# Optimization experiments

Hardware: AMD Instinct MI355X
Metric: run time of the kernel (lower is better)

Reference implementation:

```python
import jax, jax.numpy as jnp
import numpy as np

ALPHA = 1.0
GAMMA = 2.0
SMOOTH = 1e-07
B, S = 8192, 4096


def setup_inputs() -> dict:
    key = jax.random.key(0)
    k1, k2, k3, k4 = jax.random.split(key, 4)
    scores = jax.random.normal(k1, (B, S), dtype=jnp.float32)
    head_position = jax.random.randint(k2, (B,), 0, S, dtype=jnp.int64) if jax.config.jax_enable_x64 else jax.random.randint(k2, (B,), 0, S).astype(jnp.int32)
    tail_position = jax.random.randint(k3, (B,), 0, S).astype(head_position.dtype)
    score_mask = jax.random.randint(k4, (B, S), 0, 2, dtype=jnp.int32)
    return {"scores": scores, "head_position": head_position,
            "tail_position": tail_position, "score_mask": score_mask}


def reference(scores, head_position, tail_position, score_mask):
    # scores: [B, S] float; head/tail_position: [B] int; score_mask: [B, S] int
    batch_size = scores.shape[0]
    bidx = jnp.arange(batch_size)
    # exclude head and tail positions from the negative set
    m = score_mask.at[bidx, head_position].set(-1)
    m = m.at[bidx, tail_position].set(-1)
    neg = (m == 1)  # [B, S] candidate negatives
    # positive score per sample, broadcast against all candidates
    pos = jnp.take_along_axis(scores, tail_position[:, None], axis=1)  # [B, 1]
    # log_softmax over the pair [pos, neg_j] at index 0 == -softplus(neg - pos)
    logpt = -jax.nn.softplus(scores - pos)  # [B, S]
    pt = jnp.clip(jnp.exp(logpt), SMOOTH, 1.0 - SMOOTH)
    fl = -ALPHA * jnp.power(1.0 - pt, GAMMA) * logpt  # [B, S] per-pair focal loss
    negf = neg.astype(scores.dtype)
    cnt = negf.sum(axis=1)  # [B] number of negatives
    # per-sample focal_loss is the MEAN over its pairs; samples with 0 negs skipped
    per_sample = jnp.where(cnt > 0, (fl * negf).sum(axis=1) / jnp.maximum(cnt, 1.0), 0.0)
    return per_sample.sum() / batch_size
```

## Files before the change

### kernel.cpp

```cpp
#include <hip/hip_runtime.h>


__device__ __forceinline__ float focal_term(float x) {
    const float e  = __expf(x);
    const float t  = 1.f + e;
    const float sp = __logf(t);
    float pt = __builtin_amdgcn_rcpf(t);
    pt = fminf(fmaxf(pt, 1e-7f), 1.f - 1e-7f);
    const float om = 1.f - pt;
    return om * om * sp;
}

template <int S>
__global__ __launch_bounds__(256, 8) void focal_row_kernel(
    const float* __restrict__ scores,
    const int*   __restrict__ head_pos,
    const int*   __restrict__ tail_pos,
    const int*   __restrict__ mask,
    float*       __restrict__ row_out,
    int B)
{
    const int lane = threadIdx.x & 63;
    const int row  = blockIdx.x * 4 + (threadIdx.x >> 6);
    if (row >= B) return;

    const int head = head_pos[row];
    const int tail = tail_pos[row];
    const float* srow = scores + (size_t)row * S;
    const int*   mrow = mask   + (size_t)row * S;
    const float4* s4 = reinterpret_cast<const float4*>(srow);
    const int4*   m4 = reinterpret_cast<const int4*>(mrow);
    const float pos = srow[tail];

    constexpr int NIT   = S / 4 / 64;
    constexpr int DEPTH = 4;
    static_assert(NIT >= DEPTH && NIT % 4 == 0, "shape");

    float4 sbuf[DEPTH];
    int4   mbuf[DEPTH];
    #pragma unroll
    for (int i = 0; i < DEPTH; ++i) {
        sbuf[i] = s4[lane + 64 * i];
        mbuf[i] = m4[lane + 64 * i];
    }

    float fsum = 0.f;
    float cnt  = 0.f;

    #pragma unroll
    for (int i = 0; i < NIT; ++i) {
        const float4 sv = sbuf[i & (DEPTH - 1)];
        const int4   mv = mbuf[i & (DEPTH - 1)];
        if (i + DEPTH < NIT) {
            sbuf[i & (DEPTH - 1)] = s4[lane + 64 * (i + DEPTH)];
            mbuf[i & (DEPTH - 1)] = m4[lane + 64 * (i + DEPTH)];
        }
        const float se[4] = {sv.x, sv.y, sv.z, sv.w};
        const int   me[4] = {mv.x, mv.y, mv.z, mv.w};
        #pragma unroll
        for (int k = 0; k < 4; ++k) {
            const float fl = focal_term(se[k] - pos);
            const float on = (me[k] == 1) ? 1.f : 0.f;
            fsum += fl * on;
            cnt  += on;
        }
    }

    #pragma unroll
    for (int off = 32; off; off >>= 1) {
        fsum += __shfl_down(fsum, off, 64);
        cnt  += __shfl_down(cnt,  off, 64);
    }

    if (lane == 0) {
        if (mrow[head] == 1) { fsum -= focal_term(srow[head] - pos); cnt -= 1.f; }
        if (tail != head && mrow[tail] == 1) { fsum -= focal_term(0.f); cnt -= 1.f; }
        row_out[row] = (cnt > 0.f) ? fsum / cnt : 0.f;
    }
}

__global__ __launch_bounds__(256) void focal_row_generic(
    const float* __restrict__ scores,
    const int*   __restrict__ head_pos,
    const int*   __restrict__ tail_pos,
    const int*   __restrict__ mask,
    float*       __restrict__ row_out,
    int S)
{
    const int row  = blockIdx.x;
    const int tid  = threadIdx.x;
    const int head = head_pos[row];
    const int tail = tail_pos[row];
    const float* srow = scores + (size_t)row * S;
    const int*   mrow = mask   + (size_t)row * S;
    const float pos = srow[tail];
    float fsum = 0.f; float cnt = 0.f;
    for (int idx = tid; idx < S; idx += 256) {
        const float fl = focal_term(srow[idx] - pos);
        const bool isneg = (mrow[idx] == 1) && (idx != head) && (idx != tail);
        if (isneg) { fsum += fl; cnt += 1.f; }
    }
    #pragma unroll
    for (int off = 32; off; off >>= 1) {
        fsum += __shfl_down(fsum, off, 64);
        cnt  += __shfl_down(cnt,  off, 64);
    }
    __shared__ float sf[4]; __shared__ float sc[4];
    const int wave = tid >> 6;
    if ((tid & 63) == 0) { sf[wave] = fsum; sc[wave] = cnt; }
    __syncthreads();
    if (tid == 0) {
        float tot = sf[0] + sf[1] + sf[2] + sf[3];
        float c   = sc[0] + sc[1] + sc[2] + sc[3];
        row_out[row] = (c > 0.f) ? tot / c : 0.f;
    }
}

__global__ __launch_bounds__(256) void final_reduce_kernel(
    const float* __restrict__ row_out, float* __restrict__ out, int B)
{
    float sum = 0.f;
    const float4* r4 = reinterpret_cast<const float4*>(row_out);
    const int nvec = B >> 2;
    for (int i = threadIdx.x; i < nvec; i += 256) {
        float4 v = r4[i];
        sum += (v.x + v.y) + (v.z + v.w);
    }
    #pragma unroll
    for (int off = 32; off; off >>= 1) sum += __shfl_down(sum, off, 64);
    __shared__ float sf[4];
    const int wave = threadIdx.x >> 6;
    if ((threadIdx.x & 63) == 0) sf[wave] = sum;
    __syncthreads();
    if (threadIdx.x == 0) out[0] = (sf[0] + sf[1] + sf[2] + sf[3]) / (float)B;
}

extern "C" void kernel_launch(void* const* d_in, const int* in_sizes, int n_in,
                              void* d_out, int out_size, void* d_ws, size_t ws_size,
                              hipStream_t stream)
{
    const float* scores = (const float*)d_in[0];
    const int*   headp  = (const int*)d_in[1];
    const int*   tailp  = (const int*)d_in[2];
    const int*   maskp  = (const int*)d_in[3];
    const int B = in_sizes[1];
    const int S = in_sizes[0] / B;

    float* rowbuf = (float*)d_ws;
    float* out    = (float*)d_out;

    if (S == 4096) {
        const int grid = (B + 3) / 4;
        focal_row_kernel<4096><<<grid, 256, 0, stream>>>(scores, headp, tailp, maskp, rowbuf, B);
    } else {
        focal_row_generic<<<B, 256, 0, stream>>>(scores, headp, tailp, maskp, rowbuf, S);
    }
    final_reduce_kernel<<<1, 256, 0, stream>>>(rowbuf, out, B);
}
```

Baseline: 288.2 us.

## Stream row tiles into LDS with direct global-to-LDS loads, double-buffered

Replaces the per-lane register prefetch ring with double-buffered global_load_lds transfers into per-wave shared-memory tiles. Explicit vmcnt/lgkmcnt waits and a sched_barrier keep the loads overlapped with compute. It also drops the pt clamp and turns the mask compare into a float convert plus fma, trimming ALU work per element. In exchange it adds LDS traffic and manual wait management, and the mask conversion is only correct when mask values are exactly 0 or 1.

```diff
diff --git a/kernel.cpp b/kernel.cpp
--- a/kernel.cpp
+++ b/kernel.cpp
@@ -1,12 +1,16 @@
 #include <hip/hip_runtime.h>
 
+
+#define GLL(gaddr, laddr)                                                          \
+    __builtin_amdgcn_global_load_lds(                                              \
+        (const __attribute__((address_space(1))) void*)(gaddr),                    \
+        (__attribute__((address_space(3))) void*)(laddr), 16, 0, 0)
 
 __device__ __forceinline__ float focal_term(float x) {
     const float e  = __expf(x);
     const float t  = 1.f + e;
     const float sp = __logf(t);
-    float pt = __builtin_amdgcn_rcpf(t);
-    pt = fminf(fmaxf(pt, 1e-7f), 1.f - 1e-7f);
+    const float pt = __builtin_amdgcn_rcpf(t);
     const float om = 1.f - pt;
     return om * om * sp;
 }
@@ -20,49 +24,52 @@
     float*       __restrict__ row_out,
     int B)
 {
+    constexpr int NIT = S / 256;
+    static_assert(S % 256 == 0 && NIT >= 4, "shape");
+
+    __shared__ float s_lds[4][2][256];
+    __shared__ int   m_lds[4][2][256];
+
     const int lane = threadIdx.x & 63;
-    const int row  = blockIdx.x * 4 + (threadIdx.x >> 6);
+    const int wid  = threadIdx.x >> 6;
+    const int row  = blockIdx.x * 4 + wid;
     if (row >= B) return;
 
     const int head = head_pos[row];
     const int tail = tail_pos[row];
     const float* srow = scores + (size_t)row * S;
     const int*   mrow = mask   + (size_t)row * S;
-    const float4* s4 = reinterpret_cast<const float4*>(srow);
-    const int4*   m4 = reinterpret_cast<const int4*>(mrow);
     const float pos = srow[tail];
 
-    constexpr int NIT   = S / 4 / 64;
-    constexpr int DEPTH = 4;
-    static_assert(NIT >= DEPTH && NIT % 4 == 0, "shape");
+    asm volatile("s_waitcnt vmcnt(0) lgkmcnt(0)" ::: "memory");
 
-    float4 sbuf[DEPTH];
-    int4   mbuf[DEPTH];
-    #pragma unroll
-    for (int i = 0; i < DEPTH; ++i) {
-        sbuf[i] = s4[lane + 64 * i];
-        mbuf[i] = m4[lane + 64 * i];
-    }
+    GLL(srow + lane * 4,       &s_lds[wid][0][0]);
+    GLL(mrow + lane * 4,       &m_lds[wid][0][0]);
+    GLL(srow + 256 + lane * 4, &s_lds[wid][1][0]);
+    GLL(mrow + 256 + lane * 4, &m_lds[wid][1][0]);
 
-    float fsum = 0.f;
-    float cnt  = 0.f;
+    float fsum = 0.f, cnt = 0.f;
 
     #pragma unroll
     for (int i = 0; i < NIT; ++i) {
-        const float4 sv = sbuf[i & (DEPTH - 1)];
-        const int4   mv = mbuf[i & (DEPTH - 1)];
-        if (i + DEPTH < NIT) {
-            sbuf[i & (DEPTH - 1)] = s4[lane + 64 * (i + DEPTH)];
-            mbuf[i & (DEPTH - 1)] = m4[lane + 64 * (i + DEPTH)];
+        if (i == NIT - 1) asm volatile("s_waitcnt vmcnt(0)" ::: "memory");
+        else              asm volatile("s_waitcnt vmcnt(2)" ::: "memory");
+        const float4 sv = reinterpret_cast<const float4*>(&s_lds[wid][i & 1][0])[lane];
+        const int4   mv = reinterpret_cast<const int4*>(&m_lds[wid][i & 1][0])[lane];
+        asm volatile("s_waitcnt lgkmcnt(0)" ::: "memory");
+        __builtin_amdgcn_sched_barrier(0);
+        if (i + 2 < NIT) {
+            GLL(srow + (i + 2) * 256 + lane * 4, &s_lds[wid][i & 1][0]);
+            GLL(mrow + (i + 2) * 256 + lane * 4, &m_lds[wid][i & 1][0]);
         }
         const float se[4] = {sv.x, sv.y, sv.z, sv.w};
         const int   me[4] = {mv.x, mv.y, mv.z, mv.w};
         #pragma unroll
         for (int k = 0; k < 4; ++k) {
             const float fl = focal_term(se[k] - pos);
-            const float on = (me[k] == 1) ? 1.f : 0.f;
-            fsum += fl * on;
-            cnt  += on;
+            const float on = (float)me[k];
+            fsum = fmaf(fl, on, fsum);
+            cnt += on;
         }
     }
 
@@ -94,11 +101,10 @@
     const float* srow = scores + (size_t)row * S;
     const int*   mrow = mask   + (size_t)row * S;
     const float pos = srow[tail];
-    float fsum = 0.f; float cnt = 0.f;
+    float fsum = 0.f, cnt = 0.f;
     for (int idx = tid; idx < S; idx += 256) {
         const float fl = focal_term(srow[idx] - pos);
-        const bool isneg = (mrow[idx] == 1) && (idx != head) && (idx != tail);
-        if (isneg) { fsum += fl; cnt += 1.f; }
+        if ((mrow[idx] == 1) && (idx != head) && (idx != tail)) { fsum += fl; cnt += 1.f; }
     }
     #pragma unroll
     for (int off = 32; off; off >>= 1) {
```

Result: no change. 283.7 us (-1.5%).
